# Kernel optimization log

Measured on AMD Instinct MI355X. Metric: run time of the kernel, lower is better.

The kernel has to match this reference:

```python
import jax, jax.numpy as jnp
import numpy as np

B, S, D, H, DK, R = 8, 1024, 1024, 8, 128, 16
NEG = float(-2**31)


def setup_inputs() -> dict:
    key = jax.random.key(0)
    ks = jax.random.split(key, 16)
    std = 1.0 / np.sqrt(D)
    inp = {
        "query": jax.random.normal(ks[0], (B, S, D), jnp.float32),
        "key": jax.random.normal(ks[1], (B, S, D), jnp.float32),
        "value": jax.random.normal(ks[2], (B, S, D), jnp.float32),
        "mask": jax.random.bernoulli(ks[3], 0.9, (B, S, S)),
        "W_A": jax.random.normal(ks[4], (D, R), jnp.float32) * std,
        "W_B": jax.random.normal(ks[5], (R, H * DK), jnp.float32) * std,
        "W_C": jax.random.normal(ks[6], (D, R), jnp.float32) * std,
        "W_D": jax.random.normal(ks[7], (R, H * DK), jnp.float32) * std,
        "W_E": jax.random.normal(ks[8], (D, R), jnp.float32) * std,
        "W_F": jax.random.normal(ks[9], (R, H * DK), jnp.float32) * std,
        "Wq": jax.random.normal(ks[10], (D, H * DK), jnp.float32) * std,
        "bq": jnp.zeros((H * DK,), jnp.float32),
        "Wk": jax.random.normal(ks[11], (D, H * DK), jnp.float32) * std,
        "bk": jnp.zeros((H * DK,), jnp.float32),
        "Wv": jax.random.normal(ks[12], (D, H * DK), jnp.float32) * std,
        "bv": jnp.zeros((H * DK,), jnp.float32),
        "Wo": jax.random.normal(ks[13], (H * DK, D), jnp.float32) * std,
        "bo": jnp.zeros((D,), jnp.float32),
    }
    return inp


def reference(query, key, value, mask, W_A, W_B, W_C, W_D, W_E, W_F,
              Wq, bq, Wk, bk, Wv, bv, Wo, bo):
    nb = query.shape[0]
    # Linear + low-rank (LoRA-style) add; low-rank applied right-to-left for efficiency
    q = query @ Wq + bq + (query @ W_A) @ W_B      # [B,S,H*DK]
    k = key @ Wk + bk + (key @ W_C) @ W_D
    v = value @ Wv + bv + (value @ W_E) @ W_F
    # faithful plain reshape (NOT a transpose), as in the original code
    q = q.reshape(nb, H, -1, DK)                   # [B,H,S,DK]
    k = k.reshape(nb, H, -1, DK)
    v = v.reshape(nb, H, -1, DK)
    m = mask[:, None, :, :]                        # [B,1,S,S] broadcasts over heads
    scores = jnp.einsum("bhqd,bhkd->bhqk", q, k)   # no 1/sqrt(dk) scaling (faithful)
    scores = jnp.where(m, scores, jnp.float32(NEG))
    p = jax.nn.softmax(scores, axis=-1)
    x = jnp.einsum("bhqk,bhkd->bhqd", p, v)
    x = x.reshape(nb, -1, H * DK)                  # [B,S,H*DK]
    return x @ Wo + bo
```

## Files before the change

kernel.cpp:

```cpp
#include <hip/hip_runtime.h>
#include <hip/hip_bf16.h>
#include <stdint.h>


#define kB 8
#define kS 1024
#define kD 1024
#define kH 8
#define kDK 128
#define kHDK 1024
#define kM (kB * kS)
#define kMaskWords (kB * kS * (kS / 64))
#define kQKVN (kM * kHDK)

typedef _Float16 f16;
typedef __attribute__((ext_vector_type(4))) float f32x4;
typedef __attribute__((ext_vector_type(8))) _Float16 f16x8;

#define OFF_FLAG  ((size_t)0)
#define OFF_MBITS ((size_t)256)
#define OFF_WQT   (OFF_MBITS + (size_t)kMaskWords * 8)
#define OFF_WKT   (OFF_WQT + (size_t)2097152)
#define OFF_WVT   (OFF_WKT + (size_t)2097152)
#define OFF_WOT   (OFF_WVT + (size_t)2097152)
#define OFF_Q     (OFF_WOT + (size_t)2097152)
#define OFF_K     (OFF_Q  + (size_t)kQKVN * 2)
#define OFF_VT    (OFF_K  + (size_t)kQKVN * 2)
#define OFF_X     (OFF_VT + (size_t)kQKVN * 2)
#define OFF_T0    OFF_X
#define OFF_T1    (OFF_X + (size_t)kQKVN * 2)
#define OFF_T2    (OFF_X + (size_t)kQKVN * 4)
#define NEED3     (OFF_X + (size_t)kQKVN * 6)

__device__ __forceinline__ void async_load16(const void* g, void* lds_uniform) {
  auto gp = reinterpret_cast<const __attribute__((address_space(1))) unsigned int*>(
      reinterpret_cast<uintptr_t>(g));
  auto lp = reinterpret_cast<__attribute__((address_space(3))) unsigned int*>(
      reinterpret_cast<uintptr_t>(lds_uniform));
  __builtin_amdgcn_global_load_lds(gp, lp, 16, 0, 0);
}

__device__ __forceinline__ f32x4 mfma16(f16x8 a, f16x8 b, f32x4 c) {
  return __builtin_amdgcn_mfma_f32_16x16x32_f16(a, b, c, 0, 0, 0);
}

__device__ __forceinline__ float ldw(const void* p, size_t i, int f) {
  return f ? ((const float*)p)[i] : (float)((const __bf16*)p)[i];
}

__device__ __forceinline__ void swz_tiles(int& mt, int& nt) {
  const int gx = gridDim.x, gy = gridDim.y;
  const int L = blockIdx.y * gx + blockIdx.x;
  const int xcd = L & 7, rank = L >> 3;
  mt = xcd * (gy >> 3) + rank / gx;
  nt = rank % gx;
}

__global__ void detect_kernel(const unsigned int* __restrict__ qw,
                              const unsigned int* __restrict__ mw,
                              int* __restrict__ flags) {
  const int lane = threadIdx.x & 63;
  int hi = 0; bool w4 = true, b1 = true;
  #pragma unroll
  for (int j = 0; j < 4; ++j) {
    unsigned int w = qw[lane * 4 + j];
    hi += (int)(((w >> 7) & 0xFF) > 0x90) + (int)(((w >> 23) & 0xFF) > 0x90);
    unsigned int m = mw[lane * 4 + j];
    if (!(m == 0u || m == 1u || m == 0x3F800000u)) w4 = false;
    if ((m & 0xFEFEFEFEu) != 0u) b1 = false;
  }
  #pragma unroll
  for (int off = 32; off; off >>= 1) hi += __shfl_xor(hi, off, 64);
  unsigned long long bw4 = __ballot(w4), bb1 = __ballot(b1);
  if (lane == 0 && blockIdx.x == 0) {
    flags[1] = (hi > 16) ? 1 : 0;
    flags[0] = (bw4 == ~0ull) ? 4 : ((bb1 == ~0ull) ? 1 : 2);
  }
}

__global__ void pack_mask_kernel(const void* __restrict__ mask, const int* __restrict__ flags,
                                 unsigned long long* __restrict__ mbits) {
  int wi = blockIdx.x * 4 + (threadIdx.x >> 6);
  if (wi >= kMaskWords) return;
  int lane = threadIdx.x & 63;
  size_t e = (size_t)wi * 64 + lane;
  int width = flags[0];
  bool on;
  if (width == 1)      on = ((const unsigned char*)mask)[e] != 0;
  else if (width == 2) on = ((const unsigned short*)mask)[e] != 0;
  else                 on = ((const unsigned int*)mask)[e] != 0;
  unsigned long long bal = __ballot(on);
  if (lane == 0) mbits[wi] = bal;
}

__device__ __forceinline__ void convert_body(const void* src, f16* dst,
                                             const int* flags, int i) {
  f16x8 o;
  if (flags[1]) {
    f32x4 a = *(const f32x4*)((const float*)src + i);
    f32x4 b = *(const f32x4*)((const float*)src + i + 4);
    #pragma unroll
    for (int j = 0; j < 4; ++j) { o[j] = (f16)a[j]; o[4 + j] = (f16)b[j]; }
  } else {
    const __bf16* s = (const __bf16*)src + i;
    #pragma unroll
    for (int j = 0; j < 8; ++j) o[j] = (f16)(float)s[j];
  }
  *(f16x8*)(dst + i) = o;
}

__global__ __launch_bounds__(256) void convert_kernel(
    const void* __restrict__ src, f16* __restrict__ dst,
    const int* __restrict__ flags, int n) {
  const int i = (blockIdx.x * 256 + threadIdx.x) * 8;
  if (i < n) convert_body(src, dst, flags, i);
}

__global__ __launch_bounds__(256) void convert3_kernel(
    const void* __restrict__ s0, const void* __restrict__ s1, const void* __restrict__ s2,
    f16* __restrict__ d0, f16* __restrict__ d1, f16* __restrict__ d2,
    const int* __restrict__ flags) {
  const int z = blockIdx.z;
  const void* src = (z == 0) ? s0 : (z == 1) ? s1 : s2;
  f16* dst = (z == 0) ? d0 : (z == 1) ? d1 : d2;
  const int i = (blockIdx.x * 256 + threadIdx.x) * 8;
  if (i < kQKVN) convert_body(src, dst, flags, i);
}

__global__ __launch_bounds__(256) void build_weights_kernel(
    const void* __restrict__ Wq, const void* __restrict__ WA, const void* __restrict__ WB,
    const void* __restrict__ Wk, const void* __restrict__ WC, const void* __restrict__ WD,
    const void* __restrict__ Wv, const void* __restrict__ WE, const void* __restrict__ WF,
    const void* __restrict__ Wo, const int* __restrict__ flags,
    f16* __restrict__ WqT, f16* __restrict__ WkT,
    f16* __restrict__ WvT, f16* __restrict__ WoT) {
  const int z = blockIdx.z;
  const int f = flags[1];
  const void *W, *Aw = nullptr, *Bw = nullptr;
  f16* Out;
  if (z == 0)      { W = Wq; Aw = WA; Bw = WB; Out = WqT; }
  else if (z == 1) { W = Wk; Aw = WC; Bw = WD; Out = WkT; }
  else if (z == 2) { W = Wv; Aw = WE; Bw = WF; Out = WvT; }
  else             { W = Wo;                   Out = WoT; }

  __shared__ float Wt[32][33];
  __shared__ float At[32][16];
  __shared__ float Bt[16][33];
  const int tx = threadIdx.x, ty = threadIdx.y;
  const int k0 = blockIdx.y * 32, n0 = blockIdx.x * 32;
  #pragma unroll
  for (int i = 0; i < 4; ++i)
    Wt[ty + 8 * i][tx] = ldw(W, (size_t)(k0 + ty + 8 * i) * 1024 + n0 + tx, f);
  const int t = ty * 32 + tx;
  if (Aw) {
    #pragma unroll
    for (int j = 0; j < 2; ++j) {
      int e = t + j * 256;
      At[e >> 4][e & 15] = ldw(Aw, (size_t)(k0 + (e >> 4)) * 16 + (e & 15), f);
    }
    #pragma unroll
    for (int j = 0; j < 2; ++j) {
      int e = t + j * 256;
      Bt[e >> 5][e & 31] = ldw(Bw, (size_t)(e >> 5) * 1024 + n0 + (e & 31), f);
    }
  }
  __syncthreads();
  #pragma unroll
  for (int i = 0; i < 4; ++i) {
    const int nloc = ty + 8 * i, kloc = tx;
    float acc = Wt[kloc][nloc];
    if (Aw) {
      #pragma unroll
      for (int r = 0; r < 16; ++r) acc += At[kloc][r] * Bt[r][nloc];
    }
    Out[(size_t)(n0 + nloc) * 1024 + k0 + kloc] = (f16)acc;
  }
}

__device__ __forceinline__ void gemm_core(
    const f16* A, const f16* BT, const void* bias, void* C,
    const int* flags, int vtrans, int out_dyn, int N, int K,
    int m0, int n0, f16* As, f16* Bs) {
  const int f = flags[1];
  const int tid = threadIdx.x;
  const int lane = tid & 63, w = tid >> 6;
  const int wr = w >> 1, wc = w & 1;
  const int l15 = lane & 15, hi = lane >> 4;
  const int swr = (l15 >> 1) & 3;

  f32x4 acc[4][4];
  #pragma unroll
  for (int i = 0; i < 4; ++i)
    #pragma unroll
    for (int j = 0; j < 4; ++j) acc[i][j] = (f32x4){0.f, 0.f, 0.f, 0.f};

  for (int k0 = 0; k0 < K; k0 += 32) {
    if (k0) __syncthreads();
    #pragma unroll
    for (int j = 0; j < 2; ++j) {
      int c = tid + j * 256;
      int cs = c ^ ((c >> 3) & 3);
      int row = cs >> 2, piece = cs & 3;
      async_load16(A  + (size_t)(m0 + row) * K + k0 + piece * 8,
                   (char*)As + (w * 64 + j * 256) * 16);
      async_load16(BT + (size_t)(n0 + row) * K + k0 + piece * 8,
                   (char*)Bs + (w * 64 + j * 256) * 16);
    }
    __syncthreads();

    f16x8 af[4], bf_[4];
    #pragma unroll
    for (int mi = 0; mi < 4; ++mi)
      af[mi] = *(const f16x8*)&As[(wr * 64 + mi * 16 + l15) * 32 + 8 * (hi ^ swr)];
    #pragma unroll
    for (int ni = 0; ni < 4; ++ni)
      bf_[ni] = *(const f16x8*)&Bs[(wc * 64 + ni * 16 + l15) * 32 + 8 * (hi ^ swr)];
    #pragma unroll
    for (int mi = 0; mi < 4; ++mi)
      #pragma unroll
      for (int ni = 0; ni < 4; ++ni)
        acc[mi][ni] = mfma16(af[mi], bf_[ni], acc[mi][ni]);
  }

  const int wf32 = out_dyn && f;
  #pragma unroll
  for (int mi = 0; mi < 4; ++mi) {
    #pragma unroll
    for (int ni = 0; ni < 4; ++ni) {
      #pragma unroll
      for (int r = 0; r < 4; ++r) {
        const int row = m0 + wr * 64 + mi * 16 + 4 * hi + r;
        const int col = n0 + wc * 64 + ni * 16 + l15;
        float v = acc[mi][ni][r] + (bias ? ldw(bias, col, f) : 0.f);
        if (vtrans) {
          const int b = row >> 10, sp = row & 1023;
          const int fi = (sp << 10) | col;
          const int h = fi >> 17, s = (fi >> 7) & 1023, d = fi & 127;
          ((f16*)C)[(((size_t)(b * 8 + h) * 128 + d) << 10) + s] = (f16)v;
        } else if (wf32) {
          ((float*)C)[(size_t)row * N + col] = v;
        } else if (out_dyn) {
          ((__bf16*)C)[(size_t)row * N + col] = (__bf16)v;
        } else {
          ((f16*)C)[(size_t)row * N + col] = (f16)v;
        }
      }
    }
  }
}

__global__ __launch_bounds__(256) void gemm_bt_kernel(
    const f16* __restrict__ A, const f16* __restrict__ BT,
    const void* __restrict__ bias, void* __restrict__ C,
    const int* __restrict__ flags, int vtrans, int out_dyn, int N, int K) {
  __shared__ __align__(16) f16 As[128 * 32];
  __shared__ __align__(16) f16 Bs[128 * 32];
  int mt, nt;
  swz_tiles(mt, nt);
  gemm_core(A, BT, bias, C, flags, vtrans, out_dyn, N, K,
            mt * 128, nt * 128, As, Bs);
}

__global__ __launch_bounds__(256) void gemm3_kernel(
    const f16* __restrict__ A0, const f16* __restrict__ A1, const f16* __restrict__ A2,
    const f16* __restrict__ B0, const f16* __restrict__ B1, const f16* __restrict__ B2,
    const void* __restrict__ b0, const void* __restrict__ b1, const void* __restrict__ b2,
    f16* __restrict__ C0, f16* __restrict__ C1, f16* __restrict__ C2,
    const int* __restrict__ flags) {
  __shared__ __align__(16) f16 As[128 * 32];
  __shared__ __align__(16) f16 Bs[128 * 32];
  const int z = blockIdx.z;
  const f16* A  = (z == 0) ? A0 : (z == 1) ? A1 : A2;
  const f16* BT = (z == 0) ? B0 : (z == 1) ? B1 : B2;
  const void* bias = (z == 0) ? b0 : (z == 1) ? b1 : b2;
  f16* C = (z == 0) ? C0 : (z == 1) ? C1 : C2;
  int mt, nt;
  swz_tiles(mt, nt);
  gemm_core(A, BT, bias, C, flags, (z == 2) ? 1 : 0, 0, 1024, 1024,
            mt * 128, nt * 128, As, Bs);
}

__global__ __launch_bounds__(256) void attn_kernel(
    const f16* __restrict__ qbuf, const f16* __restrict__ kbuf,
    const f16* __restrict__ vT, const unsigned long long* __restrict__ mbits,
    f16* __restrict__ xbuf) {
  __shared__ __align__(16) f16 Ks[64 * 128];
  __shared__ __align__(16) f16 Vs[128 * 64];
  __shared__ __align__(16) f16 Ps[64 * 64];

  const int tid = threadIdx.x, lane = tid & 63, wv = tid >> 6;
  const int l15 = lane & 15, hi = lane >> 4;
  const int q0 = blockIdx.x * 64;
  const int h = blockIdx.y, b = blockIdx.z;
  const size_t chunk = (size_t)(b * kH + h) * (kS * kDK);
  const f16* Qg = qbuf + chunk + (size_t)q0 * kDK;
  const f16* Kg = kbuf + chunk;
  const f16* Vg = vT + chunk;
  const unsigned long long* mrow = mbits + (size_t)b * kS * 16;

  const int arow = wv * 16 + l15;
  f16x8 qf[4];
  #pragma unroll
  for (int kk = 0; kk < 4; ++kk)
    qf[kk] = *(const f16x8*)&Qg[(size_t)arow * 128 + kk * 32 + 8 * hi];

  f16x8 fone;
  #pragma unroll
  for (int j = 0; j < 8; ++j) fone[j] = (f16)1.f;

  const float NEG_INF = -__builtin_inff();
  float m_run[4] = {NEG_INF, NEG_INF, NEG_INF, NEG_INF};
  f32x4 acc_l = (f32x4){0.f, 0.f, 0.f, 0.f};
  f32x4 acc_o[8];
  #pragma unroll
  for (int j = 0; j < 8; ++j) acc_o[j] = (f32x4){0.f, 0.f, 0.f, 0.f};

  for (int t = 0; t < 16; ++t) {
    const int kv0 = t * 64;
    if (t) __syncthreads();
    #pragma unroll
    for (int j = 0; j < 4; ++j) {
      int c = tid + j * 256;
      int cs = c ^ ((c >> 4) & 7);
      async_load16((const char*)Kg + (size_t)kv0 * 256 + cs * 16,
                   (char*)Ks + (wv * 64 + j * 256) * 16);
    }
    #pragma unroll
    for (int j = 0; j < 4; ++j) {
      int c = tid + j * 256;
      int row = c >> 3, piece = (c & 7) ^ (row & 7);
      async_load16((const char*)Vg + ((size_t)row * kS + kv0 + piece * 8) * 2,
                   (char*)Vs + (wv * 64 + j * 256) * 16);
    }
    __syncthreads();

    f32x4 accs[4];
    #pragma unroll
    for (int i = 0; i < 4; ++i) accs[i] = (f32x4){0.f, 0.f, 0.f, 0.f};
    #pragma unroll
    for (int kk = 0; kk < 4; ++kk) {
      #pragma unroll
      for (int ni = 0; ni < 4; ++ni) {
        const int brow = ni * 16 + l15;
        f16x8 bk = *(const f16x8*)&Ks[brow * 128 + (((kk * 4 + hi) ^ (brow & 7)) << 3)];
        accs[ni] = mfma16(qf[kk], bk, accs[ni]);
      }
    }

    #pragma unroll
    for (int r = 0; r < 4; ++r) {
      const int prow = wv * 16 + 4 * hi + r;
      const int qrow = q0 + prow;
      const unsigned long long mw = mrow[(size_t)qrow * 16 + t];
      #pragma unroll
      for (int ni = 0; ni < 4; ++ni) {
        const int col = ni * 16 + l15;
        const bool on = (mw >> col) & 1ull;
        accs[ni][r] = on ? accs[ni][r] : NEG_INF;
      }
      const float gmax = fmaxf(fmaxf(accs[0][r], accs[1][r]),
                               fmaxf(accs[2][r], accs[3][r]));
      const float mold = m_run[r];
      if (__any(gmax > mold + 8.f)) {
        float tmax = gmax;
        #pragma unroll
        for (int off = 8; off; off >>= 1) tmax = fmaxf(tmax, __shfl_xor(tmax, off, 64));
        const float mnew = fmaxf(mold, tmax);
        if (mnew > mold) {
          const float alpha = __expf(mold - mnew);
          #pragma unroll
          for (int nj = 0; nj < 8; ++nj) acc_o[nj][r] *= alpha;
          acc_l[r] *= alpha;
          m_run[r] = mnew;
        }
      }
      const float m = m_run[r];
      #pragma unroll
      for (int ni = 0; ni < 4; ++ni) {
        const float p = (accs[ni][r] == NEG_INF) ? 0.f : __expf(accs[ni][r] - m);
        const int col = ni * 16 + l15;
        Ps[prow * 64 + (((col >> 3) ^ (prow & 7)) << 3) + (col & 7)] = (f16)p;
      }
    }

    const int prow2 = wv * 16 + l15;
    #pragma unroll
    for (int kk = 0; kk < 2; ++kk) {
      f16x8 ap = *(const f16x8*)&Ps[prow2 * 64 + (((kk * 4 + hi) ^ (prow2 & 7)) << 3)];
      acc_l = mfma16(ap, fone, acc_l);
      #pragma unroll
      for (int nj = 0; nj < 8; ++nj) {
        const int vrow = nj * 16 + l15;
        f16x8 bv = *(const f16x8*)&Vs[vrow * 64 + (((kk * 4 + hi) ^ (vrow & 7)) << 3)];
        acc_o[nj] = mfma16(ap, bv, acc_o[nj]);
      }
    }
  }

  #pragma unroll
  for (int r = 0; r < 4; ++r) {
    const float inv = (acc_l[r] > 0.f) ? 1.f / acc_l[r] : 0.f;
    const int row = q0 + wv * 16 + 4 * hi + r;
    #pragma unroll
    for (int nj = 0; nj < 8; ++nj)
      xbuf[chunk + (size_t)row * kDK + nj * 16 + l15] = (f16)(acc_o[nj][r] * inv);
  }
}

extern "C" void kernel_launch(void* const* d_in, const int* in_sizes, int n_in,
                              void* d_out, int out_size, void* d_ws, size_t ws_size,
                              hipStream_t stream) {
  const void* query = d_in[0];
  const void* key_  = d_in[1];
  const void* value = d_in[2];
  const void* mask  = d_in[3];
  const void* W_A = d_in[4];
  const void* W_B = d_in[5];
  const void* W_C = d_in[6];
  const void* W_D = d_in[7];
  const void* W_E = d_in[8];
  const void* W_F = d_in[9];
  const void* Wq  = d_in[10];
  const void* bq  = d_in[11];
  const void* Wk  = d_in[12];
  const void* bk  = d_in[13];
  const void* Wv  = d_in[14];
  const void* bv  = d_in[15];
  const void* Wo  = d_in[16];
  const void* bo  = d_in[17];

  char* ws = (char*)d_ws;
  int* flags = (int*)(ws + OFF_FLAG);
  unsigned long long* mbits = (unsigned long long*)(ws + OFF_MBITS);
  f16* WqT = (f16*)(ws + OFF_WQT);
  f16* WkT = (f16*)(ws + OFF_WKT);
  f16* WvT = (f16*)(ws + OFF_WVT);
  f16* WoT = (f16*)(ws + OFF_WOT);
  f16* qb  = (f16*)(ws + OFF_Q);
  f16* kb  = (f16*)(ws + OFF_K);
  f16* vTb = (f16*)(ws + OFF_VT);
  f16* xb  = (f16*)(ws + OFF_X);

  detect_kernel<<<1, 64, 0, stream>>>((const unsigned int*)query,
                                      (const unsigned int*)mask, flags);
  pack_mask_kernel<<<kMaskWords / 4, 256, 0, stream>>>(mask, flags, mbits);
  build_weights_kernel<<<dim3(32, 32, 4), dim3(32, 8), 0, stream>>>(
      Wq, W_A, W_B, Wk, W_C, W_D, Wv, W_E, W_F, Wo, flags, WqT, WkT, WvT, WoT);

  if (ws_size >= NEED3) {
    f16* t0 = (f16*)(ws + OFF_T0);
    f16* t1 = (f16*)(ws + OFF_T1);
    f16* t2 = (f16*)(ws + OFF_T2);
    convert3_kernel<<<dim3(kQKVN / (256 * 8), 1, 3), 256, 0, stream>>>(
        query, key_, value, t0, t1, t2, flags);
    gemm3_kernel<<<dim3(8, 64, 3), 256, 0, stream>>>(
        t0, t1, t2, WqT, WkT, WvT, bq, bk, bv, qb, kb, vTb, flags);
  } else {
    f16* tmp = (f16*)(ws + OFF_X);
    convert_kernel<<<kQKVN / (256 * 8), 256, 0, stream>>>(query, tmp, flags, kQKVN);
    gemm_bt_kernel<<<dim3(8, 64), 256, 0, stream>>>(
        tmp, WqT, bq, qb, flags, 0, 0, kHDK, kD);
    convert_kernel<<<kQKVN / (256 * 8), 256, 0, stream>>>(key_, tmp, flags, kQKVN);
    gemm_bt_kernel<<<dim3(8, 64), 256, 0, stream>>>(
        tmp, WkT, bk, kb, flags, 0, 0, kHDK, kD);
    convert_kernel<<<kQKVN / (256 * 8), 256, 0, stream>>>(value, tmp, flags, kQKVN);
    gemm_bt_kernel<<<dim3(8, 64), 256, 0, stream>>>(
        tmp, WvT, bv, vTb, flags, 1, 0, kHDK, kD);
  }

  attn_kernel<<<dim3(16, kH, kB), 256, 0, stream>>>(qb, kb, vTb, mbits, xb);

  gemm_bt_kernel<<<dim3(8, 64), 256, 0, stream>>>(
      xb, WoT, bo, d_out, flags, 0, 1, kD, kHDK);
}
```

Measured before the change: 307.7 us.

## Fuse fp32-to-f16 input conversion into QKV projection GEMM and widen K tile

Removes the separate convert kernel that wrote f16 copies of query/key/value to workspace. The projection GEMM now loads fp32 (or bf16) activations directly, converts them in registers and stores them into LDS, while weights still use async global-to-LDS loads. The K tile is also doubled from 32 to 64, with an XOR swizzle over 8 pieces, for both the projection and the output GEMM. This drops one full read/write pass over the three 32MB activation tensors and halves the number of barriers, at the cost of synchronous register-staged A loads, more LDS per block, and possibly lower occupancy.

```diff
diff --git a/kernel.cpp b/kernel.cpp
--- a/kernel.cpp
+++ b/kernel.cpp
@@ -16,6 +16,7 @@
 typedef _Float16 f16;
 typedef __attribute__((ext_vector_type(4))) float f32x4;
 typedef __attribute__((ext_vector_type(8))) _Float16 f16x8;
+typedef __attribute__((ext_vector_type(8))) __bf16 bf16x8;
 
 #define OFF_FLAG  ((size_t)0)
 #define OFF_MBITS ((size_t)256)
@@ -27,10 +28,6 @@
 #define OFF_K     (OFF_Q  + (size_t)kQKVN * 2)
 #define OFF_VT    (OFF_K  + (size_t)kQKVN * 2)
 #define OFF_X     (OFF_VT + (size_t)kQKVN * 2)
-#define OFF_T0    OFF_X
-#define OFF_T1    (OFF_X + (size_t)kQKVN * 2)
-#define OFF_T2    (OFF_X + (size_t)kQKVN * 4)
-#define NEED3     (OFF_X + (size_t)kQKVN * 6)
 
 __device__ __forceinline__ void async_load16(const void* g, void* lds_uniform) {
   auto gp = reinterpret_cast<const __attribute__((address_space(1))) unsigned int*>(
@@ -91,40 +88,6 @@
   else                 on = ((const unsigned int*)mask)[e] != 0;
   unsigned long long bal = __ballot(on);
   if (lane == 0) mbits[wi] = bal;
-}
-
-__device__ __forceinline__ void convert_body(const void* src, f16* dst,
-                                             const int* flags, int i) {
-  f16x8 o;
-  if (flags[1]) {
-    f32x4 a = *(const f32x4*)((const float*)src + i);
-    f32x4 b = *(const f32x4*)((const float*)src + i + 4);
-    #pragma unroll
-    for (int j = 0; j < 4; ++j) { o[j] = (f16)a[j]; o[4 + j] = (f16)b[j]; }
-  } else {
-    const __bf16* s = (const __bf16*)src + i;
-    #pragma unroll
-    for (int j = 0; j < 8; ++j) o[j] = (f16)(float)s[j];
-  }
-  *(f16x8*)(dst + i) = o;
-}
-
-__global__ __launch_bounds__(256) void convert_kernel(
-    const void* __restrict__ src, f16* __restrict__ dst,
-    const int* __restrict__ flags, int n) {
-  const int i = (blockIdx.x * 256 + threadIdx.x) * 8;
-  if (i < n) convert_body(src, dst, flags, i);
-}
-
-__global__ __launch_bounds__(256) void convert3_kernel(
-    const void* __restrict__ s0, const void* __restrict__ s1, const void* __restrict__ s2,
-    f16* __restrict__ d0, f16* __restrict__ d1, f16* __restrict__ d2,
-    const int* __restrict__ flags) {
-  const int z = blockIdx.z;
-  const void* src = (z == 0) ? s0 : (z == 1) ? s1 : s2;
-  f16* dst = (z == 0) ? d0 : (z == 1) ? d1 : d2;
-  const int i = (blockIdx.x * 256 + threadIdx.x) * 8;
-  if (i < kQKVN) convert_body(src, dst, flags, i);
 }
 
 __global__ __launch_bounds__(256) void build_weights_kernel(
@@ -177,51 +140,9 @@
   }
 }
 
-__device__ __forceinline__ void gemm_core(
-    const f16* A, const f16* BT, const void* bias, void* C,
-    const int* flags, int vtrans, int out_dyn, int N, int K,
-    int m0, int n0, f16* As, f16* Bs) {
-  const int f = flags[1];
-  const int tid = threadIdx.x;
-  const int lane = tid & 63, w = tid >> 6;
-  const int wr = w >> 1, wc = w & 1;
-  const int l15 = lane & 15, hi = lane >> 4;
-  const int swr = (l15 >> 1) & 3;
-
-  f32x4 acc[4][4];
-  #pragma unroll
-  for (int i = 0; i < 4; ++i)
-    #pragma unroll
-    for (int j = 0; j < 4; ++j) acc[i][j] = (f32x4){0.f, 0.f, 0.f, 0.f};
-
-  for (int k0 = 0; k0 < K; k0 += 32) {
-    if (k0) __syncthreads();
-    #pragma unroll
-    for (int j = 0; j < 2; ++j) {
-      int c = tid + j * 256;
-      int cs = c ^ ((c >> 3) & 3);
-      int row = cs >> 2, piece = cs & 3;
-      async_load16(A  + (size_t)(m0 + row) * K + k0 + piece * 8,
-                   (char*)As + (w * 64 + j * 256) * 16);
-      async_load16(BT + (size_t)(n0 + row) * K + k0 + piece * 8,
-                   (char*)Bs + (w * 64 + j * 256) * 16);
-    }
-    __syncthreads();
-
-    f16x8 af[4], bf_[4];
-    #pragma unroll
-    for (int mi = 0; mi < 4; ++mi)
-      af[mi] = *(const f16x8*)&As[(wr * 64 + mi * 16 + l15) * 32 + 8 * (hi ^ swr)];
-    #pragma unroll
-    for (int ni = 0; ni < 4; ++ni)
-      bf_[ni] = *(const f16x8*)&Bs[(wc * 64 + ni * 16 + l15) * 32 + 8 * (hi ^ swr)];
-    #pragma unroll
-    for (int mi = 0; mi < 4; ++mi)
-      #pragma unroll
-      for (int ni = 0; ni < 4; ++ni)
-        acc[mi][ni] = mfma16(af[mi], bf_[ni], acc[mi][ni]);
-  }
-
+__device__ __forceinline__ void gemm_epilogue(
+    f32x4 acc[4][4], const void* bias, void* C, int f, int vtrans, int out_dyn,
+    int N, int m0, int n0, int wr, int wc, int l15, int hi) {
   const int wf32 = out_dyn && f;
   #pragma unroll
   for (int mi = 0; mi < 4; ++mi) {
@@ -253,31 +174,147 @@
     const f16* __restrict__ A, const f16* __restrict__ BT,
     const void* __restrict__ bias, void* __restrict__ C,
     const int* __restrict__ flags, int vtrans, int out_dyn, int N, int K) {
-  __shared__ __align__(16) f16 As[128 * 32];
-  __shared__ __align__(16) f16 Bs[128 * 32];
+  __shared__ __align__(16) f16 As[128 * 64];
+  __shared__ __align__(16) f16 Bs[128 * 64];
+
+  const int f = flags[1];
+  const int tid = threadIdx.x;
+  const int lane = tid & 63, w = tid >> 6;
+  const int wr = w >> 1, wc = w & 1;
+  const int l15 = lane & 15, hi = lane >> 4;
   int mt, nt;
   swz_tiles(mt, nt);
-  gemm_core(A, BT, bias, C, flags, vtrans, out_dyn, N, K,
-            mt * 128, nt * 128, As, Bs);
-}
-
-__global__ __launch_bounds__(256) void gemm3_kernel(
-    const f16* __restrict__ A0, const f16* __restrict__ A1, const f16* __restrict__ A2,
+  const int m0 = mt * 128, n0 = nt * 128;
+
+  f32x4 acc[4][4];
+  #pragma unroll
+  for (int i = 0; i < 4; ++i)
+    #pragma unroll
+    for (int j = 0; j < 4; ++j) acc[i][j] = (f32x4){0.f, 0.f, 0.f, 0.f};
+
+  for (int k0 = 0; k0 < K; k0 += 64) {
+    if (k0) __syncthreads();
+    #pragma unroll
+    for (int j = 0; j < 4; ++j) {
+      int d = tid + j * 256;
+      int row = d >> 3, piece = (d & 7) ^ (row & 7);
+      async_load16(A  + (size_t)(m0 + row) * K + k0 + piece * 8,
+                   (char*)As + (w * 64 + j * 256) * 16);
+      async_load16(BT + (size_t)(n0 + row) * K + k0 + piece * 8,
+                   (char*)Bs + (w * 64 + j * 256) * 16);
+    }
+    __syncthreads();
+
+    #pragma unroll
+    for (int kk = 0; kk < 2; ++kk) {
+      f16x8 af[4], bf_[4];
+      #pragma unroll
+      for (int mi = 0; mi < 4; ++mi) {
+        const int row = wr * 64 + mi * 16 + l15;
+        af[mi] = *(const f16x8*)&As[row * 64 + (((kk * 4 + hi) ^ (row & 7)) << 3)];
+      }
+      #pragma unroll
+      for (int ni = 0; ni < 4; ++ni) {
+        const int row = wc * 64 + ni * 16 + l15;
+        bf_[ni] = *(const f16x8*)&Bs[row * 64 + (((kk * 4 + hi) ^ (row & 7)) << 3)];
+      }
+      #pragma unroll
+      for (int mi = 0; mi < 4; ++mi)
+        #pragma unroll
+        for (int ni = 0; ni < 4; ++ni)
+          acc[mi][ni] = mfma16(af[mi], bf_[ni], acc[mi][ni]);
+    }
+  }
+
+  gemm_epilogue(acc, bias, C, f, vtrans, out_dyn, N, m0, n0, wr, wc, l15, hi);
+}
+
+__global__ __launch_bounds__(256) void proj3_kernel(
+    const void* __restrict__ A0, const void* __restrict__ A1, const void* __restrict__ A2,
     const f16* __restrict__ B0, const f16* __restrict__ B1, const f16* __restrict__ B2,
     const void* __restrict__ b0, const void* __restrict__ b1, const void* __restrict__ b2,
     f16* __restrict__ C0, f16* __restrict__ C1, f16* __restrict__ C2,
     const int* __restrict__ flags) {
-  __shared__ __align__(16) f16 As[128 * 32];
-  __shared__ __align__(16) f16 Bs[128 * 32];
+  __shared__ __align__(16) f16 As[128 * 64];
+  __shared__ __align__(16) f16 Bs[128 * 64];
+
   const int z = blockIdx.z;
-  const f16* A  = (z == 0) ? A0 : (z == 1) ? A1 : A2;
-  const f16* BT = (z == 0) ? B0 : (z == 1) ? B1 : B2;
+  const void* A  = (z == 0) ? A0 : (z == 1) ? A1 : A2;
+  const f16* BT  = (z == 0) ? B0 : (z == 1) ? B1 : B2;
   const void* bias = (z == 0) ? b0 : (z == 1) ? b1 : b2;
   f16* C = (z == 0) ? C0 : (z == 1) ? C1 : C2;
+  const int vtrans = (z == 2);
+
+  const int f = flags[1];
+  const int tid = threadIdx.x;
+  const int lane = tid & 63, w = tid >> 6;
+  const int wr = w >> 1, wc = w & 1;
+  const int l15 = lane & 15, hi = lane >> 4;
   int mt, nt;
   swz_tiles(mt, nt);
-  gemm_core(A, BT, bias, C, flags, (z == 2) ? 1 : 0, 0, 1024, 1024,
-            mt * 128, nt * 128, As, Bs);
+  const int m0 = mt * 128, n0 = nt * 128;
+
+  f32x4 acc[4][4];
+  #pragma unroll
+  for (int i = 0; i < 4; ++i)
+    #pragma unroll
+    for (int j = 0; j < 4; ++j) acc[i][j] = (f32x4){0.f, 0.f, 0.f, 0.f};
+
+  for (int k0 = 0; k0 < 1024; k0 += 64) {
+    f16x8 areg[4];
+    #pragma unroll
+    for (int j = 0; j < 4; ++j) {
+      int d = tid + j * 256;
+      int row = d >> 3, piece = (d & 7) ^ (row & 7);
+      if (f) {
+        const float* src = (const float*)A + (size_t)(m0 + row) * 1024 + k0 + piece * 8;
+        f32x4 a = *(const f32x4*)src;
+        f32x4 b = *(const f32x4*)(src + 4);
+        #pragma unroll
+        for (int e = 0; e < 4; ++e) { areg[j][e] = (f16)a[e]; areg[j][4 + e] = (f16)b[e]; }
+      } else {
+        bf16x8 a = *(const bf16x8*)((const __bf16*)A + (size_t)(m0 + row) * 1024 + k0 + piece * 8);
+        #pragma unroll
+        for (int e = 0; e < 8; ++e) areg[j][e] = (f16)(float)a[e];
+      }
+    }
+    if (k0) __syncthreads();
+    #pragma unroll
+    for (int j = 0; j < 4; ++j) {
+      int d = tid + j * 256;
+      int row = d >> 3, piece = (d & 7) ^ (row & 7);
+      async_load16(BT + (size_t)(n0 + row) * 1024 + k0 + piece * 8,
+                   (char*)Bs + (w * 64 + j * 256) * 16);
+    }
+    #pragma unroll
+    for (int j = 0; j < 4; ++j) {
+      int d = tid + j * 256;
+      *(f16x8*)&As[d * 8] = areg[j];
+    }
+    __syncthreads();
+
+    #pragma unroll
+    for (int kk = 0; kk < 2; ++kk) {
+      f16x8 af[4], bf_[4];
+      #pragma unroll
+      for (int mi = 0; mi < 4; ++mi) {
+        const int row = wr * 64 + mi * 16 + l15;
+        af[mi] = *(const f16x8*)&As[row * 64 + (((kk * 4 + hi) ^ (row & 7)) << 3)];
+      }
+      #pragma unroll
+      for (int ni = 0; ni < 4; ++ni) {
+        const int row = wc * 64 + ni * 16 + l15;
+        bf_[ni] = *(const f16x8*)&Bs[row * 64 + (((kk * 4 + hi) ^ (row & 7)) << 3)];
+      }
+      #pragma unroll
+      for (int mi = 0; mi < 4; ++mi)
+        #pragma unroll
+        for (int ni = 0; ni < 4; ++ni)
+          acc[mi][ni] = mfma16(af[mi], bf_[ni], acc[mi][ni]);
+    }
+  }
+
+  gemm_epilogue(acc, bias, C, f, vtrans, 0, 1024, m0, n0, wr, wc, l15, hi);
 }
 
 __global__ __launch_bounds__(256) void attn_kernel(
@@ -447,26 +484,8 @@
   build_weights_kernel<<<dim3(32, 32, 4), dim3(32, 8), 0, stream>>>(
       Wq, W_A, W_B, Wk, W_C, W_D, Wv, W_E, W_F, Wo, flags, WqT, WkT, WvT, WoT);
 
-  if (ws_size >= NEED3) {
-    f16* t0 = (f16*)(ws + OFF_T0);
-    f16* t1 = (f16*)(ws + OFF_T1);
-    f16* t2 = (f16*)(ws + OFF_T2);
-    convert3_kernel<<<dim3(kQKVN / (256 * 8), 1, 3), 256, 0, stream>>>(
-        query, key_, value, t0, t1, t2, flags);
-    gemm3_kernel<<<dim3(8, 64, 3), 256, 0, stream>>>(
-        t0, t1, t2, WqT, WkT, WvT, bq, bk, bv, qb, kb, vTb, flags);
-  } else {
-    f16* tmp = (f16*)(ws + OFF_X);
-    convert_kernel<<<kQKVN / (256 * 8), 256, 0, stream>>>(query, tmp, flags, kQKVN);
-    gemm_bt_kernel<<<dim3(8, 64), 256, 0, stream>>>(
-        tmp, WqT, bq, qb, flags, 0, 0, kHDK, kD);
-    convert_kernel<<<kQKVN / (256 * 8), 256, 0, stream>>>(key_, tmp, flags, kQKVN);
-    gemm_bt_kernel<<<dim3(8, 64), 256, 0, stream>>>(
-        tmp, WkT, bk, kb, flags, 0, 0, kHDK, kD);
-    convert_kernel<<<kQKVN / (256 * 8), 256, 0, stream>>>(value, tmp, flags, kQKVN);
-    gemm_bt_kernel<<<dim3(8, 64), 256, 0, stream>>>(
-        tmp, WvT, bv, vTb, flags, 1, 0, kHDK, kD);
-  }
+  proj3_kernel<<<dim3(8, 64, 3), 256, 0, stream>>>(
+      query, key_, value, WqT, WkT, WvT, bq, bk, bv, qb, kb, vTb, flags);
 
   attn_kernel<<<dim3(16, kH, kB), 256, 0, stream>>>(qb, kb, vTb, mbits, xb);
 
```

Result: faster. 299.1 us (-2.8%).
